# Kernel optimization log

Measured on AMD Instinct MI355X. Metric: run time of the kernel, lower is better.

Reference implementation:

```python
import jax, jax.numpy as jnp
import numpy as np

TAU_MEM = 0.02
THRESHOLD = 0.5
RESET_POTENTIAL = 0.0
SURROGATE_BETA = 4.0
LN_EPS = 1e-6

B, T, F_IN, F_OUT = 64, 1024, 512, 512


def fast_sigmoid(x, beta):
    # Continuous fast-sigmoid surrogate spike: 0.5 * (beta*x / (1 + beta*|x|)) + 0.5
    bx = beta * x
    return 0.5 * bx / (1.0 + jnp.abs(bx)) + 0.5


def setup_inputs() -> dict:
    key = jax.random.key(0)
    k1, k2, k3 = jax.random.split(key, 3)
    spikes = jax.random.uniform(k1, (B, T, F_IN), dtype=jnp.float32)
    W = jax.random.normal(k2, (F_IN, F_OUT), dtype=jnp.float32) / np.sqrt(F_IN)
    b = jnp.zeros((F_OUT,), dtype=jnp.float32)
    ln_scale = jnp.ones((F_OUT,), dtype=jnp.float32)
    ln_bias = jnp.zeros((F_OUT,), dtype=jnp.float32)
    return {"spikes": spikes, "W": W, "b": b, "ln_scale": ln_scale, "ln_bias": ln_bias}


def reference(spikes, W, b, ln_scale, ln_bias):
    # Dense projection of input spike trains: [B,T,F_in] -> [B,T,F_out]
    currents = jnp.einsum('bti,io->bto', spikes, W) + b

    alpha = jnp.exp(jnp.float32(-1.0 / TAU_MEM))

    def lif_step(v_mem, cur):
        v_mem = alpha * v_mem + (1.0 - alpha) * cur
        spike = fast_sigmoid(v_mem - THRESHOLD, SURROGATE_BETA)
        v_mem = v_mem * (1.0 - spike) + RESET_POTENTIAL * spike
        return v_mem, spike

    v0 = jnp.zeros((spikes.shape[0], W.shape[1]), dtype=currents.dtype)
    _, out = jax.lax.scan(lif_step, v0, jnp.transpose(currents, (1, 0, 2)))  # [T,B,F]
    out = jnp.transpose(out, (1, 0, 2))  # [B,T,F]

    # LayerNorm over last axis (flax defaults: eps=1e-6, scale & bias)
    mean = jnp.mean(out, axis=-1, keepdims=True)
    var = jnp.var(out, axis=-1, keepdims=True)
    out = (out - mean) * jax.lax.rsqrt(var + LN_EPS) * ln_scale + ln_bias
    return out
```

## Files before the change

kernel.cpp:

```cpp
#include <hip/hip_runtime.h>

#define THREADS 512
#define NBLK 1024

typedef _Float16 half8 __attribute__((ext_vector_type(8)));
typedef float floatx4 __attribute__((ext_vector_type(4)));

__device__ __forceinline__ unsigned int f2h(float f) {
  union { _Float16 h; unsigned short u; } v;
  v.h = (_Float16)f;
  return (unsigned int)v.u;
}

__global__ void wcvt_kernel(const float* __restrict__ W, unsigned short* __restrict__ Wt) {
  __shared__ float tile[32][33];
  const int tx = threadIdx.x, ty = threadIdx.y;
  const int nb = blockIdx.x * 32, kb = blockIdx.y * 32;
#pragma unroll
  for (int i = 0; i < 4; ++i)
    tile[ty + 8 * i][tx] = W[(size_t)(kb + ty + 8 * i) * 512 + nb + tx];
  __syncthreads();
#pragma unroll
  for (int i = 0; i < 4; ++i) {
    union { _Float16 h; unsigned short u; } v;
    v.h = (_Float16)tile[tx][ty + 8 * i];
    Wt[(size_t)(nb + ty + 8 * i) * 512 + kb + tx] = v.u;
  }
}

__global__ __launch_bounds__(THREADS, 4) void lif_fused_kernel(
    const float* __restrict__ A, const unsigned short* __restrict__ Wt,
    const float* __restrict__ bias, const float* __restrict__ lnw,
    const float* __restrict__ lnb, float* __restrict__ out) {
  __shared__ uint4 smem4[4768];
  unsigned char* smem = (unsigned char*)smem4;

  const int tid  = threadIdx.x;
  const int lane = tid & 63;
  const int wave = tid >> 6;
  const int wrow = wave >> 2;
  const int wcol = wave & 3;
  const int l15  = lane & 15;
  const int g    = lane >> 4;
  const int rowBase = blockIdx.x * 64;

  const int arow  = tid >> 3;
  const int akloc = (tid & 7) << 2;
  const int aWriteOff = 65536 + arow * 64 +
                        (((akloc >> 3) ^ ((arow >> 1) & 3)) << 4) + ((akloc & 7) << 1);
  const size_t aSrcBase = (size_t)(rowBase + arow) * 512 + akloc;

  const int sw = ((g ^ ((l15 >> 1) & 3)) << 4);
  const int aReadBase = 65536 + (wrow * 32 + l15) * 64 + sw;
  const int bReadBase = (wcol * 128 + l15) * 64 + sw;

  auto stageB = [&](int bb, int kk) {
#pragma unroll
    for (int i = 0; i < 4; ++i) {
      const int n = i * 128 + (tid >> 2);
      const int slot = (tid & 3) ^ ((n >> 1) & 3);
      const unsigned short* src = Wt + n * 512 + kk * 32 + slot * 8;
      int off = bb * 32768 + i * 8192 + wave * 1024;
      off = __builtin_amdgcn_readfirstlane(off);
      __builtin_amdgcn_global_load_lds(
          (const __attribute__((address_space(1))) void*)src,
          (__attribute__((address_space(3))) void*)(smem + off), 16, 0, 0);
    }
  };

  floatx4 acc[2][8];
#pragma unroll
  for (int m = 0; m < 2; ++m)
#pragma unroll
    for (int n = 0; n < 8; ++n)
      acc[m][n] = (floatx4){0.f, 0.f, 0.f, 0.f};

  stageB(0, 0);
  {
    float4 v = *(const float4*)(A + aSrcBase);
    uint2 p;
    p.x = f2h(v.x) | (f2h(v.y) << 16);
    p.y = f2h(v.z) | (f2h(v.w) << 16);
    *(uint2*)(smem + aWriteOff) = p;
  }
  __syncthreads();

  for (int kk = 0; kk < 16; ++kk) {
    const int bb = kk & 1;
    float4 av;
    if (kk < 15) {
      stageB(bb ^ 1, kk + 1);
      av = *(const float4*)(A + aSrcBase + (size_t)(kk + 1) * 32);
    }
    half8 a0 = *(const half8*)(smem + aReadBase + bb * 4096);
    half8 a1 = *(const half8*)(smem + aReadBase + bb * 4096 + 1024);
#pragma unroll
    for (int n = 0; n < 8; ++n) {
      half8 bf = *(const half8*)(smem + bb * 32768 + bReadBase + n * 1024);
      acc[0][n] = __builtin_amdgcn_mfma_f32_16x16x32_f16(a0, bf, acc[0][n], 0, 0, 0);
      acc[1][n] = __builtin_amdgcn_mfma_f32_16x16x32_f16(a1, bf, acc[1][n], 0, 0, 0);
    }
    if (kk < 15) {
      uint2 p;
      p.x = f2h(av.x) | (f2h(av.y) << 16);
      p.y = f2h(av.z) | (f2h(av.w) << 16);
      *(uint2*)(smem + aWriteOff + (bb ^ 1) * 4096) = p;
    }
    __syncthreads();
  }

  float bcol[8], lsc[8], lbc[8];
#pragma unroll
  for (int n = 0; n < 8; ++n) {
    const int col = wcol * 128 + n * 16 + l15;
    bcol[n] = bias[col];
    lsc[n]  = lnw[col];
    lbc[n]  = lnb[col];
  }
#pragma unroll
  for (int m = 0; m < 2; ++m)
#pragma unroll
    for (int n = 0; n < 8; ++n)
#pragma unroll
      for (int r = 0; r < 4; ++r) {
        float x  = acc[m][n][r] + bcol[n] - 0.5f;
        float bx = 4.0f * x;
        acc[m][n][r] = 0.5f * bx / (1.0f + fabsf(bx)) + 0.5f;
      }

  float rs[2][4], rq[2][4];
#pragma unroll
  for (int m = 0; m < 2; ++m)
#pragma unroll
    for (int r = 0; r < 4; ++r) {
      float s = 0.f, q = 0.f;
#pragma unroll
      for (int n = 0; n < 8; ++n) {
        float v = acc[m][n][r];
        s += v;
        q += v * v;
      }
      rs[m][r] = s;
      rq[m][r] = q;
    }
#pragma unroll
  for (int d = 1; d < 16; d <<= 1) {
#pragma unroll
    for (int m = 0; m < 2; ++m)
#pragma unroll
      for (int r = 0; r < 4; ++r) {
        rs[m][r] += __shfl_xor(rs[m][r], d, 16);
        rq[m][r] += __shfl_xor(rq[m][r], d, 16);
      }
  }

  float* redS = (float*)(smem + 73728);
  float* redQ = (float*)(smem + 74752);
  float* mv   = (float*)(smem + 75776);
  if (l15 == 0) {
#pragma unroll
    for (int m = 0; m < 2; ++m)
#pragma unroll
      for (int r = 0; r < 4; ++r) {
        const int row = wrow * 32 + m * 16 + g * 4 + r;
        redS[row * 4 + wcol] = rs[m][r];
        redQ[row * 4 + wcol] = rq[m][r];
      }
  }
  __syncthreads();
  if (tid < 64) {
    const float S = redS[tid * 4] + redS[tid * 4 + 1] + redS[tid * 4 + 2] + redS[tid * 4 + 3];
    const float Q = redQ[tid * 4] + redQ[tid * 4 + 1] + redQ[tid * 4 + 2] + redQ[tid * 4 + 3];
    const float mean = S * (1.0f / 512.0f);
    const float var  = Q * (1.0f / 512.0f) - mean * mean;
    mv[tid * 2]     = mean;
    mv[tid * 2 + 1] = rsqrtf(var + 1e-6f);
  }
  __syncthreads();

#pragma unroll
  for (int m = 0; m < 2; ++m)
#pragma unroll
    for (int r = 0; r < 4; ++r) {
      const int row  = wrow * 32 + m * 16 + g * 4 + r;
      const float mean = mv[row * 2];
      const float rstd = mv[row * 2 + 1];
      const size_t base = (size_t)(rowBase + row) * 512;
#pragma unroll
      for (int n = 0; n < 8; ++n) {
        const int col = wcol * 128 + n * 16 + l15;
        out[base + col] = (acc[m][n][r] - mean) * rstd * lsc[n] + lbc[n];
      }
    }
}

extern "C" void kernel_launch(void* const* d_in, const int* in_sizes, int n_in,
                              void* d_out, int out_size, void* d_ws, size_t ws_size,
                              hipStream_t stream) {
  const float* spikes = (const float*)d_in[0];
  const float* W      = (const float*)d_in[1];
  const float* b      = (const float*)d_in[2];
  const float* lnw    = (const float*)d_in[3];
  const float* lnb    = (const float*)d_in[4];
  float* out = (float*)d_out;
  unsigned short* Wt = (unsigned short*)d_ws;

  wcvt_kernel<<<dim3(16, 16), dim3(32, 8), 0, stream>>>(W, Wt);
  lif_fused_kernel<<<NBLK, THREADS, 0, stream>>>(spikes, Wt, b, lnw, lnb, out);
}
```

Baseline: 94.81 us.

## Use 128-row tiles with triple-buffered async LDS loads for A and W

Each block now computes 128 rows instead of 64, so half as many blocks each stream the full W. The fp32 A tile is now loaded straight into LDS with async global_load_lds, and the fp16 conversion happens on the LDS read. Single-step double buffering is replaced by a three-stage pipeline using explicit vmcnt waits and one barrier per k-step, which removes the register round-trip for A. The cost is more accumulators per wave (32 floatx4), an occupancy bound lowered to 2, and double the LDS traffic for A because it is stored as fp32.

```diff
diff --git a/kernel.cpp b/kernel.cpp
--- a/kernel.cpp
+++ b/kernel.cpp
@@ -1,16 +1,10 @@
 #include <hip/hip_runtime.h>
 
 #define THREADS 512
-#define NBLK 1024
+#define NBLK 512
 
 typedef _Float16 half8 __attribute__((ext_vector_type(8)));
 typedef float floatx4 __attribute__((ext_vector_type(4)));
-
-__device__ __forceinline__ unsigned int f2h(float f) {
-  union { _Float16 h; unsigned short u; } v;
-  v.h = (_Float16)f;
-  return (unsigned int)v.u;
-}
 
 __global__ void wcvt_kernel(const float* __restrict__ W, unsigned short* __restrict__ Wt) {
   __shared__ float tile[32][33];
@@ -28,91 +22,107 @@
   }
 }
 
-__global__ __launch_bounds__(THREADS, 4) void lif_fused_kernel(
+#define ABUF 16384
+#define BBASE 49152
+#define BBUF 32768
+
+__global__ __launch_bounds__(THREADS, 2) void lif_fused_kernel(
     const float* __restrict__ A, const unsigned short* __restrict__ Wt,
     const float* __restrict__ bias, const float* __restrict__ lnw,
     const float* __restrict__ lnb, float* __restrict__ out) {
-  __shared__ uint4 smem4[4768];
+  __shared__ uint4 smem4[9216];
   unsigned char* smem = (unsigned char*)smem4;
 
   const int tid  = threadIdx.x;
   const int lane = tid & 63;
   const int wave = tid >> 6;
-  const int wrow = wave >> 2;
-  const int wcol = wave & 3;
+  const int wrow = wave >> 1;
+  const int wcol = wave & 1;
   const int l15  = lane & 15;
   const int g    = lane >> 4;
-  const int rowBase = blockIdx.x * 64;
-
-  const int arow  = tid >> 3;
-  const int akloc = (tid & 7) << 2;
-  const int aWriteOff = 65536 + arow * 64 +
-                        (((akloc >> 3) ^ ((arow >> 1) & 3)) << 4) + ((akloc & 7) << 1);
-  const size_t aSrcBase = (size_t)(rowBase + arow) * 512 + akloc;
-
-  const int sw = ((g ^ ((l15 >> 1) & 3)) << 4);
-  const int aReadBase = 65536 + (wrow * 32 + l15) * 64 + sw;
-  const int bReadBase = (wcol * 128 + l15) * 64 + sw;
-
-  auto stageB = [&](int bb, int kk) {
+  const int rowBase = blockIdx.x * 128;
+
+  const int bslot = (tid & 3) ^ ((tid >> 3) & 3);
+  const int aslot = (tid & 7) ^ ((tid >> 3) & 7);
+  const unsigned short* bsrc = Wt + (size_t)(tid >> 2) * 512 + bslot * 8;
+  const float* asrc = A + (size_t)(rowBase + (tid >> 3)) * 512 + aslot * 4;
+
+  auto stage = [&](int buf, int kk) {
 #pragma unroll
     for (int i = 0; i < 4; ++i) {
-      const int n = i * 128 + (tid >> 2);
-      const int slot = (tid & 3) ^ ((n >> 1) & 3);
-      const unsigned short* src = Wt + n * 512 + kk * 32 + slot * 8;
-      int off = bb * 32768 + i * 8192 + wave * 1024;
+      int off = BBASE + buf * BBUF + i * 8192 + wave * 1024;
       off = __builtin_amdgcn_readfirstlane(off);
       __builtin_amdgcn_global_load_lds(
-          (const __attribute__((address_space(1))) void*)src,
+          (const __attribute__((address_space(1))) void*)(bsrc + (size_t)i * 65536 + kk * 32),
           (__attribute__((address_space(3))) void*)(smem + off), 16, 0, 0);
     }
+#pragma unroll
+    for (int j = 0; j < 2; ++j) {
+      int off = buf * ABUF + j * 8192 + wave * 1024;
+      off = __builtin_amdgcn_readfirstlane(off);
+      __builtin_amdgcn_global_load_lds(
+          (const __attribute__((address_space(1))) void*)(asrc + (size_t)j * 32768 + kk * 32),
+          (__attribute__((address_space(3))) void*)(smem + off), 16, 0, 0);
+    }
   };
 
-  floatx4 acc[2][8];
-#pragma unroll
-  for (int m = 0; m < 2; ++m)
-#pragma unroll
-    for (int n = 0; n < 8; ++n)
+  const int aRowOff = (wrow * 32 + l15) * 128;
+  const int aswz = l15 & 7;
+  const int aOff0 = ((g << 1) ^ aswz) << 4;
+  const int aOff1 = aOff0 ^ 16;
+  const int bRowOff = (wcol * 256 + l15) * 64;
+  const int bsw = (g ^ ((l15 >> 1) & 3)) << 4;
+
+  floatx4 acc[2][16];
+#pragma unroll
+  for (int m = 0; m < 2; ++m)
+#pragma unroll
+    for (int n = 0; n < 16; ++n)
       acc[m][n] = (floatx4){0.f, 0.f, 0.f, 0.f};
 
-  stageB(0, 0);
-  {
-    float4 v = *(const float4*)(A + aSrcBase);
-    uint2 p;
-    p.x = f2h(v.x) | (f2h(v.y) << 16);
-    p.y = f2h(v.z) | (f2h(v.w) << 16);
-    *(uint2*)(smem + aWriteOff) = p;
-  }
-  __syncthreads();
-
-  for (int kk = 0; kk < 16; ++kk) {
-    const int bb = kk & 1;
-    float4 av;
-    if (kk < 15) {
-      stageB(bb ^ 1, kk + 1);
-      av = *(const float4*)(A + aSrcBase + (size_t)(kk + 1) * 32);
-    }
-    half8 a0 = *(const half8*)(smem + aReadBase + bb * 4096);
-    half8 a1 = *(const half8*)(smem + aReadBase + bb * 4096 + 1024);
-#pragma unroll
-    for (int n = 0; n < 8; ++n) {
-      half8 bf = *(const half8*)(smem + bb * 32768 + bReadBase + n * 1024);
-      acc[0][n] = __builtin_amdgcn_mfma_f32_16x16x32_f16(a0, bf, acc[0][n], 0, 0, 0);
-      acc[1][n] = __builtin_amdgcn_mfma_f32_16x16x32_f16(a1, bf, acc[1][n], 0, 0, 0);
-    }
-    if (kk < 15) {
-      uint2 p;
-      p.x = f2h(av.x) | (f2h(av.y) << 16);
-      p.y = f2h(av.z) | (f2h(av.w) << 16);
-      *(uint2*)(smem + aWriteOff + (bb ^ 1) * 4096) = p;
-    }
-    __syncthreads();
-  }
-
-  float bcol[8], lsc[8], lbc[8];
-#pragma unroll
-  for (int n = 0; n < 8; ++n) {
-    const int col = wcol * 128 + n * 16 + l15;
+  stage(0, 0);
+  stage(1, 1);
+
+#pragma unroll
+  for (int k = 0; k < 16; ++k) {
+    if (k < 15) {
+      asm volatile("s_waitcnt vmcnt(6)" ::: "memory");
+    } else {
+      asm volatile("s_waitcnt vmcnt(0)" ::: "memory");
+    }
+    __builtin_amdgcn_s_barrier();
+    __builtin_amdgcn_sched_barrier(0);
+
+    const int buf = k % 3;
+    const unsigned char* abase = smem + buf * ABUF + aRowOff;
+    half8 a[2];
+#pragma unroll
+    for (int m = 0; m < 2; ++m) {
+      float4 lo = *(const float4*)(abase + m * 2048 + aOff0);
+      float4 hi = *(const float4*)(abase + m * 2048 + aOff1);
+      half8 t;
+      t[0] = (_Float16)lo.x; t[1] = (_Float16)lo.y;
+      t[2] = (_Float16)lo.z; t[3] = (_Float16)lo.w;
+      t[4] = (_Float16)hi.x; t[5] = (_Float16)hi.y;
+      t[6] = (_Float16)hi.z; t[7] = (_Float16)hi.w;
+      a[m] = t;
+    }
+    const unsigned char* bbase = smem + BBASE + buf * BBUF + bRowOff + bsw;
+#pragma unroll
+    for (int n = 0; n < 16; ++n) {
+      half8 bf = *(const half8*)(bbase + n * 1024);
+      acc[0][n] = __builtin_amdgcn_mfma_f32_16x16x32_f16(a[0], bf, acc[0][n], 0, 0, 0);
+      acc[1][n] = __builtin_amdgcn_mfma_f32_16x16x32_f16(a[1], bf, acc[1][n], 0, 0, 0);
+    }
+
+    if (k < 14) stage((k + 2) % 3, k + 2);
+  }
+  __syncthreads();
+
+  float bcol[16], lsc[16], lbc[16];
+#pragma unroll
+  for (int n = 0; n < 16; ++n) {
+    const int col = wcol * 256 + n * 16 + l15;
     bcol[n] = bias[col];
     lsc[n]  = lnw[col];
     lbc[n]  = lnb[col];
@@ -120,7 +130,7 @@
 #pragma unroll
   for (int m = 0; m < 2; ++m)
 #pragma unroll
-    for (int n = 0; n < 8; ++n)
+    for (int n = 0; n < 16; ++n)
 #pragma unroll
       for (int r = 0; r < 4; ++r) {
         float x  = acc[m][n][r] + bcol[n] - 0.5f;
@@ -135,7 +145,7 @@
     for (int r = 0; r < 4; ++r) {
       float s = 0.f, q = 0.f;
 #pragma unroll
-      for (int n = 0; n < 8; ++n) {
+      for (int n = 0; n < 16; ++n) {
         float v = acc[m][n][r];
         s += v;
         q += v * v;
@@ -154,23 +164,23 @@
       }
   }
 
-  float* redS = (float*)(smem + 73728);
-  float* redQ = (float*)(smem + 74752);
-  float* mv   = (float*)(smem + 75776);
+  float* redS = (float*)smem4;
+  float* redQ = redS + 256;
+  float* mv   = redQ + 256;
   if (l15 == 0) {
 #pragma unroll
     for (int m = 0; m < 2; ++m)
 #pragma unroll
       for (int r = 0; r < 4; ++r) {
         const int row = wrow * 32 + m * 16 + g * 4 + r;
-        redS[row * 4 + wcol] = rs[m][r];
-        redQ[row * 4 + wcol] = rq[m][r];
-      }
-  }
-  __syncthreads();
-  if (tid < 64) {
-    const float S = redS[tid * 4] + redS[tid * 4 + 1] + redS[tid * 4 + 2] + redS[tid * 4 + 3];
-    const float Q = redQ[tid * 4] + redQ[tid * 4 + 1] + redQ[tid * 4 + 2] + redQ[tid * 4 + 3];
+        redS[row * 2 + wcol] = rs[m][r];
+        redQ[row * 2 + wcol] = rq[m][r];
+      }
+  }
+  __syncthreads();
+  if (tid < 128) {
+    const float S = redS[tid * 2] + redS[tid * 2 + 1];
+    const float Q = redQ[tid * 2] + redQ[tid * 2 + 1];
     const float mean = S * (1.0f / 512.0f);
     const float var  = Q * (1.0f / 512.0f) - mean * mean;
     mv[tid * 2]     = mean;
@@ -187,8 +197,8 @@
       const float rstd = mv[row * 2 + 1];
       const size_t base = (size_t)(rowBase + row) * 512;
 #pragma unroll
-      for (int n = 0; n < 8; ++n) {
-        const int col = wcol * 128 + n * 16 + l15;
+      for (int n = 0; n < 16; ++n) {
+        const int col = wcol * 256 + n * 16 + l15;
         out[base + col] = (acc[m][n][r] - mean) * rstd * lsc[n] + lbc[n];
       }
     }
```

After: 82.36 us. 1.15x faster.
